# Performance work log

Measured on AMD Instinct MI355X. Metric: run time of the kernel, lower is better.

Reference implementation:

```python
import jax, jax.numpy as jnp
import numpy as np
import math

N_HEAD = 8
HID_K = 128
HID_Q = 128


def setup_inputs() -> dict:
    key = jax.random.key(0)
    ks = jax.random.split(key, 6)
    B, KL, QL, EK, EQ = 32, 512, 512, 1024, 1024
    OUT = 1024
    return {
        "k": jax.random.normal(ks[0], (B, KL, EK), dtype=jnp.float32),
        "q": jax.random.normal(ks[1], (B, QL, EQ), dtype=jnp.float32),
        "w_kx": jax.random.normal(ks[2], (N_HEAD, EK, HID_K), dtype=jnp.float32) / math.sqrt(EK),
        "w_qx": jax.random.normal(ks[3], (N_HEAD, EQ, HID_Q), dtype=jnp.float32) / math.sqrt(EQ),
        "proj_w": jax.random.normal(ks[4], (OUT, N_HEAD * HID_K), dtype=jnp.float32) / math.sqrt(N_HEAD * HID_K),
        "proj_b": jnp.zeros((OUT,), dtype=jnp.float32),
    }


def reference(k, q, w_kx, w_qx, proj_w, proj_b):
    # k: (B, KL, EK), q: (B, QL, EQ)
    B, KL, _ = k.shape
    QL = q.shape[1]
    # per-head projections: (H, B, L, D)  -- matches torch repeat+bmm (head-major)
    kx = jnp.einsum("bke,hed->hbkd", k, w_kx)
    qx = jnp.einsum("bqe,hed->hbqd", q, w_qx)
    # scaled dot-product scores: (H, B, QL, KL)
    score = jnp.einsum("hbqd,hbkd->hbqk", qx, kx) / math.sqrt(HID_K)
    score = jax.nn.softmax(score, axis=-1)
    # context: (H, B, QL, D)
    ctx = jnp.einsum("hbqk,hbkd->hbqd", score, kx)
    # torch: split along head-major dim0 then cat on feature dim -> (B, QL, H*D)
    ctx = jnp.transpose(ctx, (1, 2, 0, 3)).reshape(B, QL, N_HEAD * HID_K)
    out = ctx @ proj_w.T + proj_b  # (B, QL, OUT); dropout=0 is identity
    # returned score matches torch shape (H*B, QL, KL), head-major
    return out, score.reshape(N_HEAD * B, QL, KL)
```

## Files before the change

kernel.cpp:

```cpp
#include <hip/hip_runtime.h>

typedef unsigned short u16;
typedef unsigned int u32;
typedef u16 u16x4 __attribute__((ext_vector_type(4)));
typedef u16 u16x8 __attribute__((ext_vector_type(8)));
typedef short bf16x8 __attribute__((ext_vector_type(8)));
typedef float f32x4 __attribute__((ext_vector_type(4)));

static __device__ __forceinline__ u16 f2bf(float f) {
  union { float f; unsigned u; } v; v.f = f;
  unsigned r = v.u + 0x7FFFu + ((v.u >> 16) & 1u);
  return (u16)(r >> 16);
}

static __device__ __forceinline__ void gld_lds16(const u16* g, u16* l) {
  __builtin_amdgcn_global_load_lds(
      (const __attribute__((address_space(1))) u32*)g,
      (__attribute__((address_space(3))) u32*)l, 16, 0, 0);
}


template<bool OUT_F32, bool WRITE_T, bool BIAS>
__global__ __launch_bounds__(256)
void gemm_bt16(const u16* __restrict__ A, const u16* __restrict__ Bt,
               void* __restrict__ C_, u16* __restrict__ Ct,
               const float* __restrict__ bias)
{
  constexpr int LD = 1024;
  __shared__ __align__(16) u16 As[128 * 64];
  __shared__ __align__(16) u16 Bs[128 * 64];

  const int tid  = threadIdx.x;
  const int lane = tid & 63;
  const int w    = tid >> 6;
  const int wr   = w >> 1, wc = w & 1;
  const int brow = blockIdx.y * 128;
  const int bcol = blockIdx.x * 128;
  const int kgrp = lane >> 4;
  const int l16  = lane & 15;

  const int srow = tid >> 3;
  const int sc   = (tid & 7) * 8;

  f32x4 acc[4][4];
#pragma unroll
  for (int m = 0; m < 4; ++m)
#pragma unroll
    for (int n = 0; n < 4; ++n) acc[m][n] = f32x4{0.f, 0.f, 0.f, 0.f};

  for (int kt = 0; kt < 1024; kt += 64) {
    const u16* Ab = A + (long)(brow + srow) * LD + kt + sc;
    const u16* Bb = Bt + (long)(bcol + srow) * LD + kt + sc;
#pragma unroll
    for (int i = 0; i < 4; ++i) {
      gld_lds16(Ab + (long)i * 32 * LD, As + (i * 256 + tid) * 8);
      gld_lds16(Bb + (long)i * 32 * LD, Bs + (i * 256 + tid) * 8);
    }
    __syncthreads();
#pragma unroll
    for (int kk = 0; kk < 2; ++kk) {
      bf16x8 af[4], bfr[4];
#pragma unroll
      for (int m = 0; m < 4; ++m)
        af[m] = *(const bf16x8*)(As + (wr * 64 + m * 16 + l16) * 64 + kk * 32 + kgrp * 8);
#pragma unroll
      for (int n = 0; n < 4; ++n)
        bfr[n] = *(const bf16x8*)(Bs + (wc * 64 + n * 16 + l16) * 64 + kk * 32 + kgrp * 8);
#pragma unroll
      for (int m = 0; m < 4; ++m)
#pragma unroll
        for (int n = 0; n < 4; ++n)
          acc[m][n] = __builtin_amdgcn_mfma_f32_16x16x32_bf16(af[m], bfr[n], acc[m][n], 0, 0, 0);
    }
    __syncthreads();
  }

#pragma unroll
  for (int m = 0; m < 4; ++m) {
    const int gr0 = brow + wr * 64 + m * 16 + kgrp * 4;
#pragma unroll
    for (int n = 0; n < 4; ++n) {
      const int gc = bcol + wc * 64 + n * 16 + l16;
      if constexpr (OUT_F32) {
        float* C = (float*)C_;
        const float bv = BIAS ? bias[gc] : 0.0f;
#pragma unroll
        for (int j = 0; j < 4; ++j)
          C[(long)(gr0 + j) * LD + gc] = acc[m][n][j] + bv;
      } else {
        u16* C = (u16*)C_;
#pragma unroll
        for (int j = 0; j < 4; ++j)
          C[(long)(gr0 + j) * LD + gc] = f2bf(acc[m][n][j]);
        if constexpr (WRITE_T) {
          u16x4 t;
#pragma unroll
          for (int j = 0; j < 4; ++j) t[j] = f2bf(acc[m][n][j]);
          long ti = ((long)(gc >> 7) * 32 + (gr0 >> 9)) * 65536 + (long)(gc & 127) * 512 + (gr0 & 511);
          *(u16x4*)(Ct + ti) = t;
        }
      }
    }
  }
}

__global__ __launch_bounds__(256)
void attn_fused(const u16* __restrict__ qx, const u16* __restrict__ kx,
                const u16* __restrict__ kxT,
                float* __restrict__ score, u16* __restrict__ ctx)
{
  __shared__ __align__(16) u16 lds[4 * 16 * 272];
  u16 (*Ks)[136] = (u16(*)[136])lds;
  const int tid = threadIdx.x, lane = tid & 63, w = tid >> 6;
  const int bid = blockIdx.x;
  const int qt = bid & 7, hb = bid >> 3, h = hb >> 5, b = hb & 31;
  const int kgrp = lane >> 4, l16 = lane & 15;

  const u16* qrow = qx + ((long)(b * 512 + qt * 64 + w * 16 + l16)) * 1024 + h * 128 + kgrp * 8;
  bf16x8 qf[4];
#pragma unroll
  for (int kk = 0; kk < 4; ++kk) qf[kk] = *(const bf16x8*)(qrow + kk * 32);

  f32x4 acc[32];
#pragma unroll
  for (int n = 0; n < 32; ++n) acc[n] = f32x4{0.f, 0.f, 0.f, 0.f};

  const u16* kbase = kx + (long)b * 512 * 1024 + h * 128;
  for (int chunk = 0; chunk < 8; ++chunk) {
    __syncthreads();
#pragma unroll
    for (int i = 0; i < 4; ++i) {
      int idx = i * 256 + tid;
      int row = idx >> 4, c8 = idx & 15;
      *(u16x8*)(&Ks[row][c8 * 8]) =
          *(const u16x8*)(kbase + (long)(chunk * 64 + row) * 1024 + c8 * 8);
    }
    __syncthreads();
#pragma unroll
    for (int kk = 0; kk < 4; ++kk)
#pragma unroll
      for (int nl = 0; nl < 4; ++nl) {
        bf16x8 bfr = *(const bf16x8*)(&Ks[nl * 16 + l16][kk * 32 + kgrp * 8]);
        acc[chunk * 4 + nl] =
            __builtin_amdgcn_mfma_f32_16x16x32_bf16(qf[kk], bfr, acc[chunk * 4 + nl], 0, 0, 0);
      }
  }

  const float scale = 0.08838834764831845f;
#pragma unroll
  for (int j = 0; j < 4; ++j) {
    float m = -1e30f;
#pragma unroll
    for (int n = 0; n < 32; ++n) m = fmaxf(m, acc[n][j]);
    m = fmaxf(m, __shfl_xor(m, 1));
    m = fmaxf(m, __shfl_xor(m, 2));
    m = fmaxf(m, __shfl_xor(m, 4));
    m = fmaxf(m, __shfl_xor(m, 8));
    float s = 0.f;
#pragma unroll
    for (int n = 0; n < 32; ++n) {
      float e = __expf((acc[n][j] - m) * scale);
      acc[n][j] = e; s += e;
    }
    s += __shfl_xor(s, 1);
    s += __shfl_xor(s, 2);
    s += __shfl_xor(s, 4);
    s += __shfl_xor(s, 8);
    float inv = 1.0f / s;
#pragma unroll
    for (int n = 0; n < 32; ++n) acc[n][j] *= inv;
  }

  float* srow = score + ((long)hb * 512 + qt * 64 + w * 16 + kgrp * 4) * 512 + l16;
#pragma unroll
  for (int j = 0; j < 4; ++j)
#pragma unroll
    for (int n = 0; n < 32; ++n)
      srow[(long)j * 512 + n * 16] = acc[n][j];

  u16* Pw = lds + w * 16 * 272;
  f32x4 acc2[8];
#pragma unroll
  for (int n = 0; n < 8; ++n) acc2[n] = f32x4{0.f, 0.f, 0.f, 0.f};
  const u16* kxTb = kxT + (long)hb * 65536;

  for (int h2 = 0; h2 < 2; ++h2) {
    __syncthreads();
#pragma unroll
    for (int j = 0; j < 4; ++j)
#pragma unroll
      for (int nn = 0; nn < 16; ++nn)
        Pw[(kgrp * 4 + j) * 272 + l16 + nn * 16] = f2bf(acc[h2 * 16 + nn][j]);
    __syncthreads();
#pragma unroll
    for (int ks = 0; ks < 8; ++ks) {
      bf16x8 pa = *(const bf16x8*)(Pw + l16 * 272 + ks * 32 + kgrp * 8);
      const u16* bbase = kxTb + (long)l16 * 512 + h2 * 256 + ks * 32 + kgrp * 8;
#pragma unroll
      for (int n = 0; n < 8; ++n) {
        bf16x8 bb = *(const bf16x8*)(bbase + (long)n * 16 * 512);
        acc2[n] = __builtin_amdgcn_mfma_f32_16x16x32_bf16(pa, bb, acc2[n], 0, 0, 0);
      }
    }
  }

  u16* crow = ctx + ((long)(b * 512 + qt * 64 + w * 16 + kgrp * 4)) * 1024 + h * 128 + l16;
#pragma unroll
  for (int n = 0; n < 8; ++n)
#pragma unroll
    for (int j = 0; j < 4; ++j)
      crow[(long)j * 1024 + n * 16] = f2bf(acc2[n][j]);
}

__global__ __launch_bounds__(256)
void pack_bf16(const float4* __restrict__ in, u16x4* __restrict__ o)
{
  long i = (long)blockIdx.x * 256 + threadIdx.x;
  float4 v = in[i];
  u16x4 t;
  t[0] = f2bf(v.x); t[1] = f2bf(v.y); t[2] = f2bf(v.z); t[3] = f2bf(v.w);
  o[i] = t;
}

__global__ __launch_bounds__(256)
void pack_whead(const float* __restrict__ w, u16* __restrict__ wT)
{
  long i = (long)blockIdx.x * 256 + threadIdx.x;
  int n = (int)(i >> 10), e = (int)(i & 1023);
  int h = n >> 7, d = n & 127;
  wT[i] = f2bf(w[((long)h * 1024 + e) * 128 + d]);
}

extern "C" void kernel_launch(void* const* d_in, const int* in_sizes, int n_in,
                              void* d_out, int out_size, void* d_ws, size_t ws_size,
                              hipStream_t stream)
{
  const float* k      = (const float*)d_in[0];
  const float* q      = (const float*)d_in[1];
  const float* w_kx   = (const float*)d_in[2];
  const float* w_qx   = (const float*)d_in[3];
  const float* proj_w = (const float*)d_in[4];
  const float* proj_b = (const float*)d_in[5];

  float* out   = (float*)d_out;
  float* score = (float*)d_out + 16777216;

  char* ws = (char*)d_ws;
  u16* wkT = (u16*)(ws + 0);
  u16* wqT = (u16*)(ws + (2l << 20));
  u16* pwB = (u16*)(ws + (4l << 20));
  u16* kbf = (u16*)(ws + 6291456l);
  u16* qbf = (u16*)(ws + 39845888l);
  u16* kx  = (u16*)(ws + 73400320l);
  u16* qx  = (u16*)(ws + 106954752l);
  u16* kxT = (u16*)(ws + 140509184l);
  u16* ctx = kbf;

  pack_bf16<<<16384, 256, 0, stream>>>((const float4*)k, (u16x4*)kbf);
  pack_bf16<<<16384, 256, 0, stream>>>((const float4*)q, (u16x4*)qbf);
  pack_bf16<<<1024, 256, 0, stream>>>((const float4*)proj_w, (u16x4*)pwB);
  pack_whead<<<4096, 256, 0, stream>>>(w_kx, wkT);
  pack_whead<<<4096, 256, 0, stream>>>(w_qx, wqT);

  gemm_bt16<false, true, false><<<dim3(8, 128), 256, 0, stream>>>(kbf, wkT, kx, kxT, nullptr);
  gemm_bt16<false, false, false><<<dim3(8, 128), 256, 0, stream>>>(qbf, wqT, qx, nullptr, nullptr);

  attn_fused<<<2048, 256, 0, stream>>>(qx, kx, kxT, score, ctx);

  gemm_bt16<true, false, true><<<dim3(8, 128), 256, 0, stream>>>(ctx, pwB, out, nullptr, proj_b);
}
```

Measured before the change: 881.2 us.

## Fuse fp32-to-bf16 input conversion into projection GEMMs and pipeline attention K loads

```diff
diff --git a/kernel.cpp b/kernel.cpp
--- a/kernel.cpp
+++ b/kernel.cpp
@@ -20,9 +20,9 @@
 }
 
 
-template<bool OUT_F32, bool WRITE_T, bool BIAS>
+template<bool A_F32, bool OUT_F32, bool WRITE_T, bool BIAS>
 __global__ __launch_bounds__(256)
-void gemm_bt16(const u16* __restrict__ A, const u16* __restrict__ Bt,
+void gemm_bt16(const void* __restrict__ A_, const u16* __restrict__ Bt,
                void* __restrict__ C_, u16* __restrict__ Ct,
                const float* __restrict__ bias)
 {
@@ -34,8 +34,10 @@
   const int lane = tid & 63;
   const int w    = tid >> 6;
   const int wr   = w >> 1, wc = w & 1;
-  const int brow = blockIdx.y * 128;
-  const int bcol = blockIdx.x * 128;
+  const int bid  = blockIdx.x;
+  const int xcd  = bid & 7, t = bid >> 3;
+  const int bcol = (t & 7) * 128;
+  const int brow = (xcd * 16 + (t >> 3)) * 128;
   const int kgrp = lane >> 4;
   const int l16  = lane & 15;
 
@@ -49,13 +51,31 @@
     for (int n = 0; n < 4; ++n) acc[m][n] = f32x4{0.f, 0.f, 0.f, 0.f};
 
   for (int kt = 0; kt < 1024; kt += 64) {
-    const u16* Ab = A + (long)(brow + srow) * LD + kt + sc;
+    if constexpr (A_F32) {
+      const float* A = (const float*)A_;
+#pragma unroll
+      for (int i = 0; i < 4; ++i) {
+        int idx = i * 256 + tid;
+        int row = idx >> 3, c8 = idx & 7;
+        const float* src = A + (long)(brow + row) * LD + kt + c8 * 8;
+        float4 v0 = *(const float4*)(src);
+        float4 v1 = *(const float4*)(src + 4);
+        u16x8 bb;
+        bb[0] = f2bf(v0.x); bb[1] = f2bf(v0.y); bb[2] = f2bf(v0.z); bb[3] = f2bf(v0.w);
+        bb[4] = f2bf(v1.x); bb[5] = f2bf(v1.y); bb[6] = f2bf(v1.z); bb[7] = f2bf(v1.w);
+        *(u16x8*)(As + row * 64 + c8 * 8) = bb;
+      }
+    } else {
+      const u16* A = (const u16*)A_;
+      const u16* Ab = A + (long)(brow + srow) * LD + kt + sc;
+#pragma unroll
+      for (int i = 0; i < 4; ++i)
+        gld_lds16(Ab + (long)i * 32 * LD, As + (i * 256 + tid) * 8);
+    }
     const u16* Bb = Bt + (long)(bcol + srow) * LD + kt + sc;
 #pragma unroll
-    for (int i = 0; i < 4; ++i) {
-      gld_lds16(Ab + (long)i * 32 * LD, As + (i * 256 + tid) * 8);
+    for (int i = 0; i < 4; ++i)
       gld_lds16(Bb + (long)i * 32 * LD, Bs + (i * 256 + tid) * 8);
-    }
     __syncthreads();
 #pragma unroll
     for (int kk = 0; kk < 2; ++kk) {
@@ -93,27 +113,30 @@
         for (int j = 0; j < 4; ++j)
           C[(long)(gr0 + j) * LD + gc] = f2bf(acc[m][n][j]);
         if constexpr (WRITE_T) {
-          u16x4 t;
-#pragma unroll
-          for (int j = 0; j < 4; ++j) t[j] = f2bf(acc[m][n][j]);
+          u16x4 tt;
+#pragma unroll
+          for (int j = 0; j < 4; ++j) tt[j] = f2bf(acc[m][n][j]);
           long ti = ((long)(gc >> 7) * 32 + (gr0 >> 9)) * 65536 + (long)(gc & 127) * 512 + (gr0 & 511);
-          *(u16x4*)(Ct + ti) = t;
+          *(u16x4*)(Ct + ti) = tt;
         }
       }
     }
   }
 }
 
-__global__ __launch_bounds__(256)
+__global__ __launch_bounds__(256, 3)
 void attn_fused(const u16* __restrict__ qx, const u16* __restrict__ kx,
                 const u16* __restrict__ kxT,
                 float* __restrict__ score, u16* __restrict__ ctx)
 {
-  __shared__ __align__(16) u16 lds[4 * 16 * 272];
-  u16 (*Ks)[136] = (u16(*)[136])lds;
+  __shared__ __align__(16) u16 lds[2 * 64 * 136];
   const int tid = threadIdx.x, lane = tid & 63, w = tid >> 6;
   const int bid = blockIdx.x;
-  const int qt = bid & 7, hb = bid >> 3, h = hb >> 5, b = hb & 31;
+  const int xcd = bid & 7, t = bid >> 3;
+  const int qt = t & 7;
+  const int h  = xcd;
+  const int b  = t >> 3;
+  const int hb = h * 32 + b;
   const int kgrp = lane >> 4, l16 = lane & 15;
 
   const u16* qrow = qx + ((long)(b * 512 + qt * 64 + w * 16 + l16)) * 1024 + h * 128 + kgrp * 8;
@@ -126,24 +149,49 @@
   for (int n = 0; n < 32; ++n) acc[n] = f32x4{0.f, 0.f, 0.f, 0.f};
 
   const u16* kbase = kx + (long)b * 512 * 1024 + h * 128;
-  for (int chunk = 0; chunk < 8; ++chunk) {
-    __syncthreads();
+
+  {
+    u16x8 r[4];
 #pragma unroll
     for (int i = 0; i < 4; ++i) {
       int idx = i * 256 + tid;
-      int row = idx >> 4, c8 = idx & 15;
-      *(u16x8*)(&Ks[row][c8 * 8]) =
-          *(const u16x8*)(kbase + (long)(chunk * 64 + row) * 1024 + c8 * 8);
-    }
-    __syncthreads();
+      r[i] = *(const u16x8*)(kbase + (long)(idx >> 4) * 1024 + (idx & 15) * 8);
+    }
+#pragma unroll
+    for (int i = 0; i < 4; ++i) {
+      int idx = i * 256 + tid;
+      *(u16x8*)(lds + (idx >> 4) * 136 + (idx & 15) * 8) = r[i];
+    }
+  }
+  __syncthreads();
+
+  for (int c = 0; c < 8; ++c) {
+    u16x8 nxt[4];
+    if (c < 7) {
+#pragma unroll
+      for (int i = 0; i < 4; ++i) {
+        int idx = i * 256 + tid;
+        nxt[i] = *(const u16x8*)(kbase + (long)((c + 1) * 64 + (idx >> 4)) * 1024 + (idx & 15) * 8);
+      }
+    }
+    const u16* Kb = lds + (c & 1) * 8704;
 #pragma unroll
     for (int kk = 0; kk < 4; ++kk)
 #pragma unroll
       for (int nl = 0; nl < 4; ++nl) {
-        bf16x8 bfr = *(const bf16x8*)(&Ks[nl * 16 + l16][kk * 32 + kgrp * 8]);
-        acc[chunk * 4 + nl] =
-            __builtin_amdgcn_mfma_f32_16x16x32_bf16(qf[kk], bfr, acc[chunk * 4 + nl], 0, 0, 0);
-      }
+        bf16x8 bfr = *(const bf16x8*)(Kb + (nl * 16 + l16) * 136 + kk * 32 + kgrp * 8);
+        acc[c * 4 + nl] =
+            __builtin_amdgcn_mfma_f32_16x16x32_bf16(qf[kk], bfr, acc[c * 4 + nl], 0, 0, 0);
+      }
+    if (c < 7) {
+      u16* Kn = lds + ((c + 1) & 1) * 8704;
+#pragma unroll
+      for (int i = 0; i < 4; ++i) {
+        int idx = i * 256 + tid;
+        *(u16x8*)(Kn + (idx >> 4) * 136 + (idx & 15) * 8) = nxt[i];
+      }
+    }
+    __syncthreads();
   }
 
   const float scale = 0.08838834764831845f;
@@ -171,18 +219,12 @@
     for (int n = 0; n < 32; ++n) acc[n][j] *= inv;
   }
 
-  float* srow = score + ((long)hb * 512 + qt * 64 + w * 16 + kgrp * 4) * 512 + l16;
-#pragma unroll
-  for (int j = 0; j < 4; ++j)
-#pragma unroll
-    for (int n = 0; n < 32; ++n)
-      srow[(long)j * 512 + n * 16] = acc[n][j];
-
   u16* Pw = lds + w * 16 * 272;
   f32x4 acc2[8];
 #pragma unroll
   for (int n = 0; n < 8; ++n) acc2[n] = f32x4{0.f, 0.f, 0.f, 0.f};
   const u16* kxTb = kxT + (long)hb * 65536;
+  float* srow = score + ((long)hb * 512 + qt * 64 + w * 16 + kgrp * 4) * 512 + l16;
 
   for (int h2 = 0; h2 < 2; ++h2) {
     __syncthreads();
@@ -192,6 +234,11 @@
       for (int nn = 0; nn < 16; ++nn)
         Pw[(kgrp * 4 + j) * 272 + l16 + nn * 16] = f2bf(acc[h2 * 16 + nn][j]);
     __syncthreads();
+#pragma unroll
+    for (int j = 0; j < 4; ++j)
+#pragma unroll
+      for (int nn = 0; nn < 16; ++nn)
+        srow[(long)j * 512 + (h2 * 16 + nn) * 16] = acc[h2 * 16 + nn][j];
 #pragma unroll
     for (int ks = 0; ks < 8; ++ks) {
       bf16x8 pa = *(const bf16x8*)(Pw + l16 * 272 + ks * 32 + kgrp * 8);
@@ -249,23 +296,19 @@
   u16* wkT = (u16*)(ws + 0);
   u16* wqT = (u16*)(ws + (2l << 20));
   u16* pwB = (u16*)(ws + (4l << 20));
-  u16* kbf = (u16*)(ws + 6291456l);
-  u16* qbf = (u16*)(ws + 39845888l);
-  u16* kx  = (u16*)(ws + 73400320l);
-  u16* qx  = (u16*)(ws + 106954752l);
-  u16* kxT = (u16*)(ws + 140509184l);
-  u16* ctx = kbf;
-
-  pack_bf16<<<16384, 256, 0, stream>>>((const float4*)k, (u16x4*)kbf);
-  pack_bf16<<<16384, 256, 0, stream>>>((const float4*)q, (u16x4*)qbf);
+  u16* kx  = (u16*)(ws + 6291456l);
+  u16* qx  = (u16*)(ws + 39845888l);
+  u16* kxT = (u16*)(ws + 73400320l);
+  u16* ctx = (u16*)(ws + 106954752l);
+
   pack_bf16<<<1024, 256, 0, stream>>>((const float4*)proj_w, (u16x4*)pwB);
   pack_whead<<<4096, 256, 0, stream>>>(w_kx, wkT);
   pack_whead<<<4096, 256, 0, stream>>>(w_qx, wqT);
 
-  gemm_bt16<false, true, false><<<dim3(8, 128), 256, 0, stream>>>(kbf, wkT, kx, kxT, nullptr);
-  gemm_bt16<false, false, false><<<dim3(8, 128), 256, 0, stream>>>(qbf, wqT, qx, nullptr, nullptr);
+  gemm_bt16<true, false, true, false><<<1024, 256, 0, stream>>>(k, wkT, kx, kxT, nullptr);
+  gemm_bt16<true, false, false, false><<<1024, 256, 0, stream>>>(q, wqT, qx, nullptr, nullptr);
 
   attn_fused<<<2048, 256, 0, stream>>>(qx, kx, kxT, score, ctx);
 
-  gemm_bt16<true, false, true><<<dim3(8, 128), 256, 0, stream>>>(ctx, pwB, out, nullptr, proj_b);
-}
+  gemm_bt16<false, true, false, true><<<1024, 256, 0, stream>>>(ctx, pwB, out, nullptr, proj_b);
+}
```

After: 835.3 us. 5.2% less time.
